# Kernel tuning notes

Hardware: AMD Instinct MI355X
Metric: run time of the kernel (lower is better)

The kernel has to match this reference:

```python
import jax, jax.numpy as jnp
import numpy as np

E = 1_600_000      # num edges
N = 50_000         # num nodes
G = 100            # num graphs in batch
EMB = 128          # emb_size
OUT = 256          # out_emb_size
NRAD = 6           # num_radial
NDENSE = 3         # num_dense


def setup_inputs() -> dict:
    key = jax.random.key(0)
    ks = jax.random.split(key, 8)
    m = jax.random.normal(ks[0], (E, EMB), dtype=jnp.float32)
    rbf = jax.random.normal(ks[1], (E, NRAD), dtype=jnp.float32)
    src = jax.random.randint(ks[2], (E,), 0, N, dtype=jnp.int64)
    graph_ids = jnp.sort(jax.random.randint(ks[3], (N,), 0, G, dtype=jnp.int64))
    # parameters (torch Linear convention: W [out, in])
    W_rbf = jax.random.normal(ks[4], (EMB, NRAD), dtype=jnp.float32) / np.sqrt(NRAD)
    W_up = jax.random.normal(ks[5], (OUT, EMB), dtype=jnp.float32) / np.sqrt(EMB)
    W_dense = jax.random.normal(ks[6], (NDENSE, OUT, OUT), dtype=jnp.float32) / np.sqrt(OUT)
    b_dense = jnp.zeros((NDENSE, OUT), dtype=jnp.float32)
    return {"m": m, "rbf": rbf, "src": src, "graph_ids": graph_ids,
            "W_rbf": W_rbf, "W_up": W_up, "W_dense": W_dense, "b_dense": b_dense}


def reference(m, rbf, src, graph_ids, W_rbf, W_up, W_dense, b_dense):
    # edge transform: tmp = m * dense_rbf(rbf)            [E, EMB]
    tmp = m * jnp.einsum('er,fr->ef', rbf, W_rbf)
    # reverse-graph copy_e/sum == scatter-sum onto original src nodes
    t = jax.ops.segment_sum(tmp, src, num_segments=N)     # [N, EMB]
    # up projection (no bias)
    t = jnp.einsum('ne,oe->no', t, W_up)                  # [N, OUT]
    # dense MLP with SiLU
    for i in range(NDENSE):
        t = jax.nn.silu(jnp.einsum('no,po->np', t, W_dense[i]) + b_dense[i])
    # extensive readout: per-graph sum
    out = jax.ops.segment_sum(t, graph_ids, num_segments=G)  # [G, OUT]
    return out
```

## Files before the change

kernel.cpp:

```cpp
#include <hip/hip_runtime.h>
#include <hip/hip_bf16.h>

typedef __attribute__((ext_vector_type(8))) short short8;
typedef __attribute__((ext_vector_type(4))) float f32x4;

#define EMB 128
#define OUT 256
#define NRAD 6
#define NDENSE 3
#define BSH 7
#define MAXBKT 512
#define HB 256

static __device__ __forceinline__ unsigned short f32_to_bf16(float f) {
    union { float f; unsigned u; } v; v.f = f;
    unsigned r = v.u + 0x7fffu + ((v.u >> 16) & 1u);
    return (unsigned short)(r >> 16);
}
static __device__ __forceinline__ float silu(float x) {
    return x / (1.f + __expf(-x));
}
static __device__ __forceinline__ void gload_lds16(const void* gp, void* lp) {
    __builtin_amdgcn_global_load_lds(
        (const __attribute__((address_space(1))) void*)gp,
        (__attribute__((address_space(3))) void*)lp, 16, 0, 0);
}

__global__ __launch_bounds__(256) void setup_hist_kernel(
        const int* __restrict__ src, int* __restrict__ bpart,
        const float* __restrict__ Wup, const float* __restrict__ Wd,
        unsigned short* __restrict__ Wbf, float* __restrict__ out,
        int E, int nbkt, int outn) {
    __shared__ int h[MAXBKT];
    for (int b = threadIdx.x; b < nbkt; b += 256) h[b] = 0;
    __syncthreads();
    int gtid = blockIdx.x * blockDim.x + threadIdx.x;
    int stride = gridDim.x * blockDim.x;
    for (int e = gtid; e < E; e += stride)
        atomicAdd(&h[src[e] >> BSH], 1);
    for (int j = gtid; j < outn; j += stride) out[j] = 0.f;
    const int n1 = OUT * EMB, n2 = NDENSE * OUT * OUT;
    for (int j = gtid; j < n1 + n2; j += stride)
        Wbf[j] = f32_to_bf16(j < n1 ? Wup[j] : Wd[j - n1]);
    __syncthreads();
    int* row = bpart + (size_t)blockIdx.x * MAXBKT;
    for (int b = threadIdx.x; b < nbkt; b += 256) row[b] = h[b];
}

__global__ __launch_bounds__(512) void bscan_kernel(
        const int* __restrict__ bpart, int* __restrict__ bbase,
        int* __restrict__ gcursor, int nbkt, int E) {
    __shared__ int s[MAXBKT];
    int t = threadIdx.x;
    int v = 0;
    if (t < nbkt) {
#pragma unroll 8
        for (int k = 0; k < HB; ++k) v += bpart[(size_t)k * MAXBKT + t];
    }
    s[t] = v;
    __syncthreads();
    for (int d = 1; d < MAXBKT; d <<= 1) {
        int x = (t >= d) ? s[t - d] : 0;
        __syncthreads();
        s[t] += x;
        __syncthreads();
    }
    if (t < nbkt) {
        int ex = s[t] - v;
        bbase[t] = ex;
        gcursor[t] = ex;
    }
    if (t == 0) bbase[nbkt] = E;
}

__global__ __launch_bounds__(256) void bscatter_kernel(
        const int* __restrict__ src, int* __restrict__ gcursor,
        int2* __restrict__ pairs, int E, int nbkt) {
    __shared__ int h[MAXBKT];
    __shared__ int base[MAXBKT];
    for (int b = threadIdx.x; b < nbkt; b += 256) h[b] = 0;
    __syncthreads();
    const int per = (E + gridDim.x - 1) / gridDim.x;
    const int e0 = blockIdx.x * per;
    const int e1 = min(e0 + per, E);
    for (int e = e0 + threadIdx.x; e < e1; e += 256)
        atomicAdd(&h[src[e] >> BSH], 1);
    __syncthreads();
    for (int b = threadIdx.x; b < nbkt; b += 256)
        base[b] = h[b] ? atomicAdd(&gcursor[b], h[b]) : 0;
    __syncthreads();
    for (int e = e0 + threadIdx.x; e < e1; e += 256) {
        int s = src[e];
        int pos = atomicAdd(&base[s >> BSH], 1);
        pairs[pos] = make_int2(e, s);
    }
}

__global__ __launch_bounds__(256) void local_csr_kernel(
        const int2* __restrict__ pairs, const int* __restrict__ bbase,
        int* __restrict__ offsets, int* __restrict__ perm, int N, int E, int nbkt) {
    __shared__ int cnt[128], exc[128], cur[128];
    const int b = blockIdx.x;
    const int t = threadIdx.x;
    const int n0 = b << BSH;
    const int nn = min(128, N - n0);
    const int p0 = bbase[b], p1 = bbase[b + 1];
    if (t < 128) cnt[t] = 0;
    __syncthreads();
    for (int i = p0 + t; i < p1; i += 256)
        atomicAdd(&cnt[pairs[i].y - n0], 1);
    __syncthreads();
    if (t < 128) exc[t] = cnt[t];
    __syncthreads();
    for (int d = 1; d < 128; d <<= 1) {
        int x = (t >= d && t < 128) ? exc[t - d] : 0;
        __syncthreads();
        if (t < 128) exc[t] += x;
        __syncthreads();
    }
    if (t < 128) {
        int ex = exc[t] - cnt[t];
        cur[t] = ex;
        if (t < nn) offsets[n0 + t] = p0 + ex;
    }
    if (b == 0 && t == 0) offsets[N] = E;
    __syncthreads();
    for (int i = p0 + t; i < p1; i += 256) {
        int2 pr = pairs[i];
        int pos = p0 + atomicAdd(&cur[pr.y - n0], 1);
        perm[pos] = pr.x;
    }
}

__global__ __launch_bounds__(256) void edge_accum_kernel(
        const float* __restrict__ m, const float* __restrict__ rbf,
        const int* __restrict__ perm, const int* __restrict__ offsets,
        const float* __restrict__ W_rbf, uint2* __restrict__ t_pack, int N) {
    const int lane = threadIdx.x & 63;
    const int h = lane >> 5;
    const int c = lane & 31;
    const int gw = blockIdx.x * (blockDim.x >> 6) + (threadIdx.x >> 6);
    const int nwaves = gridDim.x * (blockDim.x >> 6);

    float wk[4][6];
#pragma unroll
    for (int k = 0; k < 4; ++k)
#pragma unroll
        for (int j = 0; j < 6; ++j) wk[k][j] = W_rbf[(4 * c + k) * NRAD + j];

    for (int node = gw; node < N; node += nwaves) {
        const int beg = offsets[node], end = offsets[node + 1];
        float a0 = 0.f, a1 = 0.f, a2 = 0.f, a3 = 0.f;
        int pe = 0;
        if (beg < end) {
            int pi = beg + (lane & 31); if (pi > end - 1) pi = end - 1;
            pe = perm[pi];
        }
        for (int cb = beg; cb < end; cb += 32) {
            int pe_next = 0;
            if (cb + 32 < end) {
                int pi = cb + 32 + (lane & 31); if (pi > end - 1) pi = end - 1;
                pe_next = perm[pi];
            }
#pragma unroll
            for (int p = 0; p < 16; ++p) {
                int e = __shfl(pe, 2 * p + h);
                const float2* rp = (const float2*)(rbf + (size_t)e * NRAD);
                float2 r0 = rp[0], r1 = rp[1], r2 = rp[2];
                float4 mv = *(const float4*)(m + (size_t)e * EMB + 4 * c);
                float g = (cb + 2 * p + h < end) ? 1.f : 0.f;
                float p0 = (wk[0][0]*r0.x + wk[0][1]*r0.y + wk[0][2]*r1.x
                          + wk[0][3]*r1.y + wk[0][4]*r2.x + wk[0][5]*r2.y) * g;
                float p1 = (wk[1][0]*r0.x + wk[1][1]*r0.y + wk[1][2]*r1.x
                          + wk[1][3]*r1.y + wk[1][4]*r2.x + wk[1][5]*r2.y) * g;
                float p2 = (wk[2][0]*r0.x + wk[2][1]*r0.y + wk[2][2]*r1.x
                          + wk[2][3]*r1.y + wk[2][4]*r2.x + wk[2][5]*r2.y) * g;
                float p3 = (wk[3][0]*r0.x + wk[3][1]*r0.y + wk[3][2]*r1.x
                          + wk[3][3]*r1.y + wk[3][4]*r2.x + wk[3][5]*r2.y) * g;
                a0 = fmaf(mv.x, p0, a0);
                a1 = fmaf(mv.y, p1, a1);
                a2 = fmaf(mv.z, p2, a2);
                a3 = fmaf(mv.w, p3, a3);
            }
            pe = pe_next;
        }
        a0 += __shfl_xor(a0, 32);
        a1 += __shfl_xor(a1, 32);
        a2 += __shfl_xor(a2, 32);
        a3 += __shfl_xor(a3, 32);
        if (h == 0) {
            uint2 pk;
            pk.x = (unsigned)f32_to_bf16(a0) | ((unsigned)f32_to_bf16(a1) << 16);
            pk.y = (unsigned)f32_to_bf16(a2) | ((unsigned)f32_to_bf16(a3) << 16);
            t_pack[(size_t)node * 32 + c] = pk;
        }
    }
}

__global__ __launch_bounds__(256) void fused_mlp2_kernel(
        const unsigned short* __restrict__ A0,
        const unsigned short* __restrict__ Wup,
        const unsigned short* __restrict__ Wd,
        const float* __restrict__ bd,
        const int* __restrict__ gids,
        float* __restrict__ out, int M) {
    __shared__ char Abuf[32768];
    __shared__ char Wbuf[32768];
    const int t    = threadIdx.x;
    const int w    = t >> 6;
    const int lane = t & 63;
    const int r    = lane & 15;
    const int g    = lane >> 4;
    const int row0 = blockIdx.x * 64;

    f32x4 acc[4][4];

#pragma unroll
    for (int it = 0; it < 4; ++it) {
        int unit = it * 256 + t;
        int row  = unit >> 4;
        int seg  = unit & 15;
        int csrc = (seg * 16) ^ ((row & 7) << 4);
        int ga = row0 + row; if (ga >= M) ga = M - 1;
        gload_lds16((const char*)A0 + (size_t)ga * 256 + csrc, Abuf + unit * 16);
    }

#pragma unroll
    for (int i = 0; i < 4; ++i)
#pragma unroll
        for (int j = 0; j < 4; ++j) acc[i][j] = (f32x4){0.f, 0.f, 0.f, 0.f};
#pragma unroll
    for (int kci = 0; kci < 2; ++kci) {
        const int kc = kci * 64;
        if (kci) __syncthreads();
#pragma unroll
        for (int it = 0; it < 8; ++it) {
            int unit = it * 256 + t;
            int wrow = unit >> 3;
            int seg  = unit & 7;
            int csrc = (seg * 16) ^ ((wrow & 7) << 4);
            gload_lds16((const char*)Wup + (size_t)wrow * 256 + kc * 2 + csrc,
                        Wbuf + unit * 16);
        }
        asm volatile("s_waitcnt vmcnt(0)" ::: "memory");
        __syncthreads();
#pragma unroll
        for (int ks = 0; ks < 2; ++ks) {
            short8 af[4], bf[4];
#pragma unroll
            for (int mi = 0; mi < 4; ++mi) {
                int row = mi * 16 + r;
                int off = kc * 2 + ks * 64 + g * 16;
                af[mi] = *(const short8*)(Abuf + row * 256 + (off ^ ((row & 7) << 4)));
            }
#pragma unroll
            for (int nj = 0; nj < 4; ++nj) {
                int col = w * 64 + nj * 16 + r;
                bf[nj] = *(const short8*)(Wbuf + col * 128
                          + ((ks * 64 + g * 16) ^ ((col & 7) << 4)));
            }
#pragma unroll
            for (int mi = 0; mi < 4; ++mi)
#pragma unroll
                for (int nj = 0; nj < 4; ++nj)
                    acc[mi][nj] = __builtin_amdgcn_mfma_f32_16x16x32_bf16(
                        af[mi], bf[nj], acc[mi][nj], 0, 0, 0);
        }
    }
    __syncthreads();
#pragma unroll
    for (int mi = 0; mi < 4; ++mi)
#pragma unroll
        for (int nj = 0; nj < 4; ++nj)
#pragma unroll
            for (int q = 0; q < 4; ++q) {
                int row = mi * 16 + g * 4 + q;
                int col = w * 64 + nj * 16 + r;
                *(unsigned short*)(Abuf + row * 512 + ((col * 2) ^ ((row & 7) << 4)))
                    = f32_to_bf16(acc[mi][nj][q]);
            }
    __syncthreads();

    for (int ell = 0; ell < NDENSE; ++ell) {
        const unsigned short* Wl = Wd + (size_t)ell * OUT * OUT;
        const float* bias = bd + ell * OUT;
#pragma unroll
        for (int i = 0; i < 4; ++i)
#pragma unroll
            for (int j = 0; j < 4; ++j) acc[i][j] = (f32x4){0.f, 0.f, 0.f, 0.f};
#pragma unroll
        for (int kci = 0; kci < 4; ++kci) {
            const int kc = kci * 64;
            __syncthreads();
#pragma unroll
            for (int it = 0; it < 8; ++it) {
                int unit = it * 256 + t;
                int wrow = unit >> 3;
                int seg  = unit & 7;
                int csrc = (seg * 16) ^ ((wrow & 7) << 4);
                gload_lds16((const char*)Wl + (size_t)wrow * 512 + kc * 2 + csrc,
                            Wbuf + unit * 16);
            }
            asm volatile("s_waitcnt vmcnt(0)" ::: "memory");
            __syncthreads();
#pragma unroll
            for (int ks = 0; ks < 2; ++ks) {
                short8 af[4], bf[4];
#pragma unroll
                for (int mi = 0; mi < 4; ++mi) {
                    int row = mi * 16 + r;
                    int off = kc * 2 + ks * 64 + g * 16;
                    af[mi] = *(const short8*)(Abuf + row * 512 + (off ^ ((row & 7) << 4)));
                }
#pragma unroll
                for (int nj = 0; nj < 4; ++nj) {
                    int col = w * 64 + nj * 16 + r;
                    bf[nj] = *(const short8*)(Wbuf + col * 128
                              + ((ks * 64 + g * 16) ^ ((col & 7) << 4)));
                }
#pragma unroll
                for (int mi = 0; mi < 4; ++mi)
#pragma unroll
                    for (int nj = 0; nj < 4; ++nj)
                        acc[mi][nj] = __builtin_amdgcn_mfma_f32_16x16x32_bf16(
                            af[mi], bf[nj], acc[mi][nj], 0, 0, 0);
            }
        }
        __syncthreads();
        if (ell < NDENSE - 1) {
#pragma unroll
            for (int mi = 0; mi < 4; ++mi)
#pragma unroll
                for (int nj = 0; nj < 4; ++nj) {
                    int col = w * 64 + nj * 16 + r;
                    float b = bias[col];
#pragma unroll
                    for (int q = 0; q < 4; ++q) {
                        int row = mi * 16 + g * 4 + q;
                        *(unsigned short*)(Abuf + row * 512
                            + ((col * 2) ^ ((row & 7) << 4)))
                            = f32_to_bf16(silu(acc[mi][nj][q] + b));
                    }
                }
            __syncthreads();
        } else {
            bool uni = (row0 + 63 < M) && (gids[row0] == gids[row0 + 63]);
            if (uni) {
                int gph = gids[row0];
                float* og = out + (size_t)gph * OUT;
#pragma unroll
                for (int nj = 0; nj < 4; ++nj) {
                    int gcol = w * 64 + nj * 16 + r;
                    float b = bias[gcol];
                    float s = 0.f;
#pragma unroll
                    for (int mi = 0; mi < 4; ++mi)
#pragma unroll
                        for (int q = 0; q < 4; ++q)
                            s += silu(acc[mi][nj][q] + b);
                    s += __shfl_xor(s, 16);
                    s += __shfl_xor(s, 32);
                    if (g == 0) atomicAdd(&og[gcol], s);
                }
            } else {
#pragma unroll
                for (int nj = 0; nj < 4; ++nj) {
                    int gcol = w * 64 + nj * 16 + r;
                    float b = bias[gcol];
#pragma unroll
                    for (int mi = 0; mi < 4; ++mi)
#pragma unroll
                        for (int q = 0; q < 4; ++q) {
                            int grow = row0 + mi * 16 + g * 4 + q;
                            if (grow < M)
                                atomicAdd(&out[(size_t)gids[grow] * OUT + gcol],
                                          silu(acc[mi][nj][q] + b));
                        }
                }
            }
        }
    }
}

extern "C" void kernel_launch(void* const* d_in, const int* in_sizes, int n_in,
                              void* d_out, int out_size, void* d_ws, size_t ws_size,
                              hipStream_t stream) {
    const float* m         = (const float*)d_in[0];
    const float* rbf       = (const float*)d_in[1];
    const int*   src       = (const int*)d_in[2];
    const int*   gids      = (const int*)d_in[3];
    const float* W_rbf     = (const float*)d_in[4];
    const float* W_up      = (const float*)d_in[5];
    const float* W_dense   = (const float*)d_in[6];
    const float* b_dense   = (const float*)d_in[7];
    float* out = (float*)d_out;

    const int E = in_sizes[2];
    const int N = in_sizes[3];
    const int nbkt = (N + 127) >> BSH;

    size_t off = 0;
    auto alloc = [&](size_t bytes) -> void* {
        void* p = (char*)d_ws + off;
        off += (bytes + 255) & ~(size_t)255;
        return p;
    };
    int* bpart   = (int*)alloc((size_t)HB * MAXBKT * 4);
    int* bbase   = (int*)alloc((size_t)(MAXBKT + 1) * 4);
    int* gcursor = (int*)alloc((size_t)MAXBKT * 4);
    int* offsets = (int*)alloc(((size_t)N + 1) * 4);
    int2* pairs  = (int2*)alloc((size_t)E * 8);
    int* perm    = (int*)alloc((size_t)E * 4);
    unsigned short* t_bf = (unsigned short*)alloc((size_t)N * EMB * 2);
    unsigned short* Wbf  = (unsigned short*)alloc((size_t)(OUT * EMB + NDENSE * OUT * OUT) * 2);
    unsigned short* Wup_bf = Wbf;
    unsigned short* Wd_bf  = Wbf + OUT * EMB;

    setup_hist_kernel<<<HB, 256, 0, stream>>>(src, bpart, W_up, W_dense, Wbf,
                                              out, E, nbkt, out_size);
    bscan_kernel<<<1, MAXBKT, 0, stream>>>(bpart, bbase, gcursor, nbkt, E);
    bscatter_kernel<<<512, 256, 0, stream>>>(src, gcursor, pairs, E, nbkt);
    local_csr_kernel<<<nbkt, 256, 0, stream>>>(pairs, bbase, offsets, perm, N, E, nbkt);

    edge_accum_kernel<<<2048, 256, 0, stream>>>(m, rbf, perm, offsets, W_rbf,
                                                (uint2*)t_bf, N);

    fused_mlp2_kernel<<<(N + 63) / 64, 256, 0, stream>>>(t_bf, Wup_bf, Wd_bf,
                                                         b_dense, gids, out, N);
}
```

Before: 423.1 us.

## Pack CSR pairs into one int, halve MLP weight tiles, cut histogram blocks

The bucket scatter now stores each edge as a single int (edge index shifted left, plus the low 7 bits of the node id) instead of an int2, halving pairs traffic in bscatter and local_csr. The fused MLP kernel loads weight tiles of 32 K-columns in a new unswizzled layout, indexed by lane group, halving Wbuf LDS so more blocks can share a CU, but it now takes twice as many sync-separated K steps. It also drops two barriers after the activation writes and halves the histogram grid (HB 256 to 128). Packing assumes E<<7 fits in an int, and the new Wbuf layout may cause LDS bank conflicts.

```diff
diff --git a/kernel.cpp b/kernel.cpp
--- a/kernel.cpp
+++ b/kernel.cpp
@@ -10,7 +10,7 @@
 #define NDENSE 3
 #define BSH 7
 #define MAXBKT 512
-#define HB 256
+#define HB 128
 
 static __device__ __forceinline__ unsigned short f32_to_bf16(float f) {
     union { float f; unsigned u; } v; v.f = f;
@@ -75,7 +75,7 @@
 
 __global__ __launch_bounds__(256) void bscatter_kernel(
         const int* __restrict__ src, int* __restrict__ gcursor,
-        int2* __restrict__ pairs, int E, int nbkt) {
+        int* __restrict__ pairs, int E, int nbkt) {
     __shared__ int h[MAXBKT];
     __shared__ int base[MAXBKT];
     for (int b = threadIdx.x; b < nbkt; b += 256) h[b] = 0;
@@ -92,12 +92,12 @@
     for (int e = e0 + threadIdx.x; e < e1; e += 256) {
         int s = src[e];
         int pos = atomicAdd(&base[s >> BSH], 1);
-        pairs[pos] = make_int2(e, s);
+        pairs[pos] = (e << BSH) | (s & ((1 << BSH) - 1));
     }
 }
 
 __global__ __launch_bounds__(256) void local_csr_kernel(
-        const int2* __restrict__ pairs, const int* __restrict__ bbase,
+        const int* __restrict__ pairs, const int* __restrict__ bbase,
         int* __restrict__ offsets, int* __restrict__ perm, int N, int E, int nbkt) {
     __shared__ int cnt[128], exc[128], cur[128];
     const int b = blockIdx.x;
@@ -108,7 +108,7 @@
     if (t < 128) cnt[t] = 0;
     __syncthreads();
     for (int i = p0 + t; i < p1; i += 256)
-        atomicAdd(&cnt[pairs[i].y - n0], 1);
+        atomicAdd(&cnt[pairs[i] & 127], 1);
     __syncthreads();
     if (t < 128) exc[t] = cnt[t];
     __syncthreads();
@@ -126,9 +126,9 @@
     if (b == 0 && t == 0) offsets[N] = E;
     __syncthreads();
     for (int i = p0 + t; i < p1; i += 256) {
-        int2 pr = pairs[i];
-        int pos = p0 + atomicAdd(&cur[pr.y - n0], 1);
-        perm[pos] = pr.x;
+        int pr = pairs[i];
+        int pos = p0 + atomicAdd(&cur[pr & 127], 1);
+        perm[pos] = pr >> BSH;
     }
 }
 
@@ -205,7 +205,7 @@
         const int* __restrict__ gids,
         float* __restrict__ out, int M) {
     __shared__ char Abuf[32768];
-    __shared__ char Wbuf[32768];
+    __shared__ char Wbuf[16384];
     const int t    = threadIdx.x;
     const int w    = t >> 6;
     const int lane = t & 63;
@@ -230,42 +230,33 @@
 #pragma unroll
         for (int j = 0; j < 4; ++j) acc[i][j] = (f32x4){0.f, 0.f, 0.f, 0.f};
 #pragma unroll
-    for (int kci = 0; kci < 2; ++kci) {
-        const int kc = kci * 64;
+    for (int kci = 0; kci < 4; ++kci) {
+        const int kc = kci * 32;
         if (kci) __syncthreads();
 #pragma unroll
-        for (int it = 0; it < 8; ++it) {
-            int unit = it * 256 + t;
-            int wrow = unit >> 3;
-            int seg  = unit & 7;
-            int csrc = (seg * 16) ^ ((wrow & 7) << 4);
-            gload_lds16((const char*)Wup + (size_t)wrow * 256 + kc * 2 + csrc,
-                        Wbuf + unit * 16);
-        }
+        for (int it = 0; it < 4; ++it)
+            gload_lds16((const char*)Wup + (size_t)t * 256 + kc * 2 + it * 16,
+                        Wbuf + it * 4096 + t * 16);
         asm volatile("s_waitcnt vmcnt(0)" ::: "memory");
         __syncthreads();
-#pragma unroll
-        for (int ks = 0; ks < 2; ++ks) {
-            short8 af[4], bf[4];
-#pragma unroll
-            for (int mi = 0; mi < 4; ++mi) {
-                int row = mi * 16 + r;
-                int off = kc * 2 + ks * 64 + g * 16;
-                af[mi] = *(const short8*)(Abuf + row * 256 + (off ^ ((row & 7) << 4)));
-            }
-#pragma unroll
-            for (int nj = 0; nj < 4; ++nj) {
-                int col = w * 64 + nj * 16 + r;
-                bf[nj] = *(const short8*)(Wbuf + col * 128
-                          + ((ks * 64 + g * 16) ^ ((col & 7) << 4)));
-            }
-#pragma unroll
-            for (int mi = 0; mi < 4; ++mi)
-#pragma unroll
-                for (int nj = 0; nj < 4; ++nj)
-                    acc[mi][nj] = __builtin_amdgcn_mfma_f32_16x16x32_bf16(
-                        af[mi], bf[nj], acc[mi][nj], 0, 0, 0);
-        }
+        short8 af[4], bf[4];
+#pragma unroll
+        for (int mi = 0; mi < 4; ++mi) {
+            int row = mi * 16 + r;
+            int off = kc * 2 + g * 16;
+            af[mi] = *(const short8*)(Abuf + row * 256 + (off ^ ((row & 7) << 4)));
+        }
+#pragma unroll
+        for (int nj = 0; nj < 4; ++nj) {
+            int col = w * 64 + nj * 16 + r;
+            bf[nj] = *(const short8*)(Wbuf + g * 4096 + col * 16);
+        }
+#pragma unroll
+        for (int mi = 0; mi < 4; ++mi)
+#pragma unroll
+            for (int nj = 0; nj < 4; ++nj)
+                acc[mi][nj] = __builtin_amdgcn_mfma_f32_16x16x32_bf16(
+                    af[mi], bf[nj], acc[mi][nj], 0, 0, 0);
     }
     __syncthreads();
 #pragma unroll
@@ -279,7 +270,6 @@
                 *(unsigned short*)(Abuf + row * 512 + ((col * 2) ^ ((row & 7) << 4)))
                     = f32_to_bf16(acc[mi][nj][q]);
             }
-    __syncthreads();
 
     for (int ell = 0; ell < NDENSE; ++ell) {
         const unsigned short* Wl = Wd + (size_t)ell * OUT * OUT;
@@ -289,42 +279,33 @@
 #pragma unroll
             for (int j = 0; j < 4; ++j) acc[i][j] = (f32x4){0.f, 0.f, 0.f, 0.f};
 #pragma unroll
-        for (int kci = 0; kci < 4; ++kci) {
-            const int kc = kci * 64;
+        for (int kci = 0; kci < 8; ++kci) {
+            const int kc = kci * 32;
             __syncthreads();
 #pragma unroll
-            for (int it = 0; it < 8; ++it) {
-                int unit = it * 256 + t;
-                int wrow = unit >> 3;
-                int seg  = unit & 7;
-                int csrc = (seg * 16) ^ ((wrow & 7) << 4);
-                gload_lds16((const char*)Wl + (size_t)wrow * 512 + kc * 2 + csrc,
-                            Wbuf + unit * 16);
-            }
+            for (int it = 0; it < 4; ++it)
+                gload_lds16((const char*)Wl + (size_t)t * 512 + kc * 2 + it * 16,
+                            Wbuf + it * 4096 + t * 16);
             asm volatile("s_waitcnt vmcnt(0)" ::: "memory");
             __syncthreads();
-#pragma unroll
-            for (int ks = 0; ks < 2; ++ks) {
-                short8 af[4], bf[4];
-#pragma unroll
-                for (int mi = 0; mi < 4; ++mi) {
-                    int row = mi * 16 + r;
-                    int off = kc * 2 + ks * 64 + g * 16;
-                    af[mi] = *(const short8*)(Abuf + row * 512 + (off ^ ((row & 7) << 4)));
-                }
-#pragma unroll
-                for (int nj = 0; nj < 4; ++nj) {
-                    int col = w * 64 + nj * 16 + r;
-                    bf[nj] = *(const short8*)(Wbuf + col * 128
-                              + ((ks * 64 + g * 16) ^ ((col & 7) << 4)));
-                }
-#pragma unroll
-                for (int mi = 0; mi < 4; ++mi)
-#pragma unroll
-                    for (int nj = 0; nj < 4; ++nj)
-                        acc[mi][nj] = __builtin_amdgcn_mfma_f32_16x16x32_bf16(
-                            af[mi], bf[nj], acc[mi][nj], 0, 0, 0);
-            }
+            short8 af[4], bf[4];
+#pragma unroll
+            for (int mi = 0; mi < 4; ++mi) {
+                int row = mi * 16 + r;
+                int off = kc * 2 + g * 16;
+                af[mi] = *(const short8*)(Abuf + row * 512 + (off ^ ((row & 7) << 4)));
+            }
+#pragma unroll
+            for (int nj = 0; nj < 4; ++nj) {
+                int col = w * 64 + nj * 16 + r;
+                bf[nj] = *(const short8*)(Wbuf + g * 4096 + col * 16);
+            }
+#pragma unroll
+            for (int mi = 0; mi < 4; ++mi)
+#pragma unroll
+                for (int nj = 0; nj < 4; ++nj)
+                    acc[mi][nj] = __builtin_amdgcn_mfma_f32_16x16x32_bf16(
+                        af[mi], bf[nj], acc[mi][nj], 0, 0, 0);
         }
         __syncthreads();
         if (ell < NDENSE - 1) {
@@ -342,7 +323,6 @@
                             = f32_to_bf16(silu(acc[mi][nj][q] + b));
                     }
                 }
-            __syncthreads();
         } else {
             bool uni = (row0 + 63 < M) && (gids[row0] == gids[row0 + 63]);
             if (uni) {
@@ -409,7 +389,7 @@
     int* bbase   = (int*)alloc((size_t)(MAXBKT + 1) * 4);
     int* gcursor = (int*)alloc((size_t)MAXBKT * 4);
     int* offsets = (int*)alloc(((size_t)N + 1) * 4);
-    int2* pairs  = (int2*)alloc((size_t)E * 8);
+    int* pairs   = (int*)alloc((size_t)E * 4);
     int* perm    = (int*)alloc((size_t)E * 4);
     unsigned short* t_bf = (unsigned short*)alloc((size_t)N * EMB * 2);
     unsigned short* Wbf  = (unsigned short*)alloc((size_t)(OUT * EMB + NDENSE * OUT * OUT) * 2);
```

New measurement: 462.8 us. 9.4% more time.
